# Optimization experiments

Hardware: AMD Instinct MI355X
Metric: run time of the kernel (lower is better)

The kernel has to match this reference:

```python
import jax, jax.numpy as jnp
import numpy as np

NUM_ENT = 100000
NUM_REL = 500            # distinct relations; table holds 2*NUM_REL (forward + inverse)
E = 500000               # total edges: first half original, second half reversed
D = 200                  # init_dim = gcn_dim = embed_dim
B = 256
KW, KH = 10, 20          # ConvE reshape: 2*KW*KH == 2*D
NF, KS = 200, 7
FLAT = (2 * KW - KS + 1) * (KH - KS + 1) * NF  # 14*14*200 = 39200
EPS = 1e-5


def setup_inputs() -> dict:
    key = jax.random.key(0)
    k = jax.random.split(key, 24)
    half = E // 2
    src = jax.random.randint(k[0], (half,), 0, NUM_ENT)
    dst = jax.random.randint(k[1], (half,), 0, NUM_ENT)
    et = jax.random.randint(k[2], (half,), 0, NUM_REL)
    edge_index = jnp.stack([jnp.concatenate([src, dst]), jnp.concatenate([dst, src])])
    edge_type = jnp.concatenate([et, et + NUM_REL])
    sub = jax.random.randint(k[3], (B,), 0, NUM_ENT)
    rel = jax.random.randint(k[4], (B,), 0, 2 * NUM_REL)
    g = lambda i, shape, s=0.05: jax.random.normal(k[i], shape, jnp.float32) * s
    return dict(
        sub=sub, rel=rel, edge_index=edge_index, edge_type=edge_type,
        init_embed=g(5, (NUM_ENT, D)), init_rel=g(6, (2 * NUM_REL, D)),
        loop_rel1=g(7, (1, D)), loop_rel2=g(8, (1, D)),
        w_in1=g(9, (D, D)), w_out1=g(10, (D, D)), w_loop1=g(11, (D, D)), w_rel1=g(12, (D, D)), b1=jnp.zeros((D,), jnp.float32),
        w_in2=g(13, (D, D)), w_out2=g(14, (D, D)), w_loop2=g(15, (D, D)), w_rel2=g(16, (D, D)), b2=jnp.zeros((D,), jnp.float32),
        conv_w=g(17, (NF, 1, KS, KS)), conv_b=jnp.zeros((NF,), jnp.float32),
        bn0_g=jnp.ones((1,), jnp.float32), bn0_b=jnp.zeros((1,), jnp.float32),
        bn1_g=jnp.ones((NF,), jnp.float32), bn1_b=jnp.zeros((NF,), jnp.float32),
        bn2_g=jnp.ones((D,), jnp.float32), bn2_b=jnp.zeros((D,), jnp.float32),
        fc_w=g(18, (FLAT, D)), fc_b=jnp.zeros((D,), jnp.float32),
        ent_bias=jnp.zeros((NUM_ENT,), jnp.float32),
    )


def _bn2d(x, g, b):  # eval-mode BN: running mean 0, running var 1
    s = g / jnp.sqrt(1.0 + EPS)
    return x * s[None, :, None, None] + b[None, :, None, None]


def _bn1d(x, g, b):
    return x * (g / jnp.sqrt(1.0 + EPS)) + b


def _agg(x_src, rel_e, dst, w):
    # message = comp(h_src, h_rel) @ W   (subtraction composition), degree-normalized scatter
    m = (x_src - rel_e) @ w                                        # [E/2, D]
    s = jax.ops.segment_sum(m, dst, num_segments=NUM_ENT)          # [N, D]
    deg = jax.ops.segment_sum(jnp.ones(dst.shape, m.dtype), dst, num_segments=NUM_ENT)
    return s / jnp.clip(deg, 1.0)[:, None]


def _ragcn_layer(x, r, ei, et, w_in, w_out, w_loop, w_rel, loop_rel, b):
    half = ei.shape[1] // 2
    src, dst = ei[0], ei[1]
    re = r[et]                                                     # [E, D]
    res = (_agg(x[src[:half]], re[:half], dst[:half], w_in)
           + _agg(x[src[half:]], re[half:], dst[half:], w_out)
           + (x - loop_rel) @ w_loop)
    return jnp.tanh(res / 3.0 + b), r @ w_rel


def _forward(sub, rel, edge_index, edge_type, init_embed, init_rel,
             loop_rel1, loop_rel2, w_in1, w_out1, w_loop1, w_rel1, b1,
             w_in2, w_out2, w_loop2, w_rel2, b2, conv_w, conv_b,
             bn0_g, bn0_b, bn1_g, bn1_b, bn2_g, bn2_b, fc_w, fc_b, ent_bias):
    x, r = _ragcn_layer(init_embed, init_rel, edge_index, edge_type, w_in1, w_out1, w_loop1, w_rel1, loop_rel1, b1)
    x, r = _ragcn_layer(x, r, edge_index, edge_type, w_in2, w_out2, w_loop2, w_rel2, loop_rel2, b2)
    sub_emb = x[sub]                                               # [B, D]
    rel_emb = r[rel]                                               # [B, D]
    # ConvE concat: [B,2,D] -> [B,D,2] -> [B,1,2*KW,KH]
    stk = jnp.transpose(jnp.stack([sub_emb, rel_emb], axis=1), (0, 2, 1)).reshape(-1, 1, 2 * KW, KH)
    h = _bn2d(stk, bn0_g, bn0_b)
    h = jax.lax.conv_general_dilated(h, conv_w, (1, 1), 'VALID',
                                     dimension_numbers=('NCHW', 'OIHW', 'NCHW'))
    h = h + conv_b[None, :, None, None]
    h = jax.nn.relu(_bn2d(h, bn1_g, bn1_b))
    h = h.reshape(-1, FLAT)
    h = h @ fc_w + fc_b
    h = jax.nn.relu(_bn1d(h, bn2_g, bn2_b))
    logits = h @ x.T + ent_bias                                    # [B, NUM_ENT]
    return jax.nn.sigmoid(logits)


def reference(sub, rel, edge_index, edge_type, init_embed, init_rel,
              loop_rel1, loop_rel2, w_in1, w_out1, w_loop1, w_rel1, b1,
              w_in2, w_out2, w_loop2, w_rel2, b2, conv_w, conv_b,
              bn0_g, bn0_b, bn1_g, bn1_b, bn2_g, bn2_b, fc_w, fc_b, ent_bias):
    return _forward(sub, rel, edge_index, edge_type, init_embed, init_rel,
                    loop_rel1, loop_rel2, w_in1, w_out1, w_loop1, w_rel1, b1,
                    w_in2, w_out2, w_loop2, w_rel2, b2, conv_w, conv_b,
                    bn0_g, bn0_b, bn1_g, bn1_b, bn2_g, bn2_b, fc_w, fc_b, ent_bias)
```

## Files before the change

### kernel.cpp

```cpp
#include <hip/hip_runtime.h>
#include <math.h>

#define N_ENT   100000
#define N_REL2  1000
#define E_TOT   500000
#define E_HALF  250000
#define DIM     200
#define BB      256
#define NFILT   200
#define FLATK   39200
#define EPS_BN  1e-5f

#define NROWS   200000
#define SCHUNK  2048
#define SNBLK   ((NROWS + SCHUNK - 1) / SCHUNK)

#define FC_KC   175
#define FC_KLEN 224

typedef __attribute__((ext_vector_type(8))) short bf16x8;
typedef __attribute__((ext_vector_type(4))) float f32x4;

__device__ __forceinline__ unsigned short f2b(float f) {
    union { float f; unsigned u; } c; c.f = f;
    unsigned u = c.u;
    u += 0x7fffu + ((u >> 16) & 1u);
    return (unsigned short)(u >> 16);
}
__device__ __forceinline__ float b2f(unsigned short h) {
    union { unsigned u; float f; } c; c.u = ((unsigned)h) << 16;
    return c.f;
}
__device__ __forceinline__ float fast_tanh(float x) {
    float ax = fabsf(x);
    float e = __expf(-2.0f * ax);
    float t = (1.0f - e) / (1.0f + e);
    return copysignf(t, x);
}

__global__ void convert_kernel(const float* __restrict__ s, unsigned short* __restrict__ d,
                               int n) {
    int i = (blockIdx.x * 256 + threadIdx.x) * 4;
    if (i + 3 < n) {
        float4 v = *(const float4*)(s + i);
        ushort4 o;
        o.x = f2b(v.x); o.y = f2b(v.y); o.z = f2b(v.z); o.w = f2b(v.w);
        *(ushort4*)(d + i) = o;
    } else {
        for (; i < n; ++i) d[i] = f2b(s[i]);
    }
}

__global__ void wstack_kernel(const float* __restrict__ wIn, const float* __restrict__ wOut,
                              const float* __restrict__ wLoop, unsigned short* __restrict__ WTK) {
    int g = blockIdx.x * 256 + threadIdx.x;
    if (g >= 3 * 28 * 224 * 8) return;
    int kk = g & 7;
    int t = g >> 3;
    int col = t % 224;
    int t2 = t / 224;
    int unit = t2 % 28;
    int seg = t2 / 28;
    int k = unit * 8 + kk;
    float v = 0.f;
    if (col < 200 && k < 200)
        v = (seg == 0 ? wIn : seg == 1 ? wOut : wLoop)[k * 200 + col];
    WTK[g] = f2b(v);
}

__global__ void fwt_kernel(const float* __restrict__ fw, unsigned short* __restrict__ FWT) {
    __shared__ float t[32][33];
    const int bid = blockIdx.x;
    const int kt = bid % 1225, jt = bid / 1225;
    const int tid = threadIdx.x;
#pragma unroll
    for (int it = 0; it < 4; ++it) {
        int idx = tid + it * 256;
        int kk = idx >> 5, jj = idx & 31;
        int j = jt * 32 + jj;
        t[kk][jj] = (j < 200) ? fw[(size_t)(kt * 32 + kk) * 200 + j] : 0.f;
    }
    __syncthreads();
#pragma unroll
    for (int it = 0; it < 4; ++it) {
        int idx = tid + it * 256;
        int jj = idx >> 5, kk = idx & 31;
        int j = jt * 32 + jj;
        if (j < 208)
            FWT[(size_t)j * FLATK + kt * 32 + kk] = f2b(t[kk][jj]);
    }
}

__global__ void hist_kernel(const int* __restrict__ ei, int* __restrict__ cnt) {
    int e = blockIdx.x * 256 + threadIdx.x;
    if (e >= E_TOT) return;
    int row = ei[E_TOT + e] + (e < E_HALF ? 0 : N_ENT);
    atomicAdd(&cnt[row], 1);
}

__global__ void scan1_kernel(const int* __restrict__ cnt, int* __restrict__ row_start,
                             int* __restrict__ blockSum) {
    __shared__ int tsum[256];
    const int t = threadIdx.x;
    const int base = blockIdx.x * SCHUNK + t * 8;
    int v[8];
    int s = 0;
#pragma unroll
    for (int i = 0; i < 8; ++i) {
        int idx = base + i;
        int c = (idx < NROWS) ? cnt[idx] : 0;
        v[i] = s;
        s += c;
    }
    tsum[t] = s;
    __syncthreads();
    for (int off = 1; off < 256; off <<= 1) {
        int x = (t >= off) ? tsum[t - off] : 0;
        __syncthreads();
        if (t >= off) tsum[t] += x;
        __syncthreads();
    }
    int texc = (t == 0) ? 0 : tsum[t - 1];
    if (t == 0) blockSum[blockIdx.x] = tsum[255];
#pragma unroll
    for (int i = 0; i < 8; ++i) {
        int idx = base + i;
        if (idx < NROWS) row_start[idx] = texc + v[i];
    }
}

__global__ void scan2_kernel(int* __restrict__ blockSum) {
    int s = 0;
    for (int i = 0; i < SNBLK; ++i) { int c = blockSum[i]; blockSum[i] = s; s += c; }
}

__global__ void scan3_kernel(int* __restrict__ row_start, int* __restrict__ row_cur,
                             const int* __restrict__ blockSum) {
    int i = blockIdx.x * 256 + threadIdx.x;
    if (i >= NROWS) return;
    int v = row_start[i] + blockSum[i / SCHUNK];
    row_start[i] = v;
    row_cur[i] = v;
}

__global__ void fill_kernel(const int* __restrict__ ei, const int* __restrict__ et,
                            int* __restrict__ row_cur, int2* __restrict__ epair) {
    int e = blockIdx.x * 256 + threadIdx.x;
    if (e >= E_TOT) return;
    int row = ei[E_TOT + e] + (e < E_HALF ? 0 : N_ENT);
    int pos = atomicAdd(&row_cur[row], 1);
    epair[pos] = make_int2(ei[e], et[e]);
}

__global__ void gather_kernel(const unsigned short* __restrict__ x,
                              const unsigned short* __restrict__ r,
                              const int2* __restrict__ epair,
                              const int* __restrict__ row_start, const int* __restrict__ cnt,
                              unsigned short* __restrict__ agg) {
    int wid = blockIdx.x * 4 + (threadIdx.x >> 6);
    if (wid >= NROWS) return;
    int lane = threadIdx.x & 63;
    if (lane >= 50) return;
    int start = row_start[wid];
    int deg = cnt[wid];
    float a0 = 0.f, a1 = 0.f, a2 = 0.f, a3 = 0.f;
    float c0 = 0.f, c1 = 0.f, c2 = 0.f, c3 = 0.f;
    int i = 0;
    for (; i + 2 <= deg; i += 2) {
        int2 e0 = epair[start + i];
        int2 e1 = epair[start + i + 1];
        ushort4 xv0 = *(const ushort4*)(x + (size_t)e0.x * DIM + lane * 4);
        ushort4 rv0 = *(const ushort4*)(r + (size_t)e0.y * DIM + lane * 4);
        ushort4 xv1 = *(const ushort4*)(x + (size_t)e1.x * DIM + lane * 4);
        ushort4 rv1 = *(const ushort4*)(r + (size_t)e1.y * DIM + lane * 4);
        a0 += b2f(xv0.x) - b2f(rv0.x);
        a1 += b2f(xv0.y) - b2f(rv0.y);
        a2 += b2f(xv0.z) - b2f(rv0.z);
        a3 += b2f(xv0.w) - b2f(rv0.w);
        c0 += b2f(xv1.x) - b2f(rv1.x);
        c1 += b2f(xv1.y) - b2f(rv1.y);
        c2 += b2f(xv1.z) - b2f(rv1.z);
        c3 += b2f(xv1.w) - b2f(rv1.w);
    }
    if (i < deg) {
        int2 e = epair[start + i];
        ushort4 xv = *(const ushort4*)(x + (size_t)e.x * DIM + lane * 4);
        ushort4 rv = *(const ushort4*)(r + (size_t)e.y * DIM + lane * 4);
        a0 += b2f(xv.x) - b2f(rv.x);
        a1 += b2f(xv.y) - b2f(rv.y);
        a2 += b2f(xv.z) - b2f(rv.z);
        a3 += b2f(xv.w) - b2f(rv.w);
    }
    float sc = 1.0f / fmaxf((float)deg, 1.0f);
    ushort4 o;
    o.x = f2b((a0 + c0) * sc);
    o.y = f2b((a1 + c1) * sc);
    o.z = f2b((a2 + c2) * sc);
    o.w = f2b((a3 + c3) * sc);
    *(ushort4*)(agg + (size_t)wid * DIM + lane * 4) = o;
}

__global__ void lv_kernel(const float* __restrict__ lr, const float* __restrict__ wl,
                          float* __restrict__ lv) {
    int j = blockIdx.x * blockDim.x + threadIdx.x;
    if (j >= DIM) return;
    float acc = 0.f;
    for (int k = 0; k < DIM; ++k) acc += lr[k] * wl[k * DIM + j];
    lv[j] = acc;
}

__global__ void rgemm_kernel(const float* __restrict__ r, const float* __restrict__ w,
                             float* __restrict__ out, int rows) {
    int g = blockIdx.x * 256 + threadIdx.x;
    if (g >= rows * DIM) return;
    int i = g / DIM, j = g - i * DIM;
    float acc = 0.f;
    for (int k = 0; k < DIM; ++k) acc += r[i * DIM + k] * w[k * DIM + j];
    out[g] = acc;
}

#define LOAD_A2(g, buf) do {                                                    \
    const unsigned short* Ap_ = Aseg[(g) / 7];                                  \
    const unsigned short* base_ = Ap_ + (size_t)arow * 200 + ((g) % 7) * 32 + lq * 8; \
    buf[0] = *(const bf16x8*)(base_);                                           \
    buf[1] = *(const bf16x8*)(base_ + 16 * 200);                                \
} while (0)

__global__ __launch_bounds__(256, 4) void layer_mfma_kernel(
        const unsigned short* __restrict__ aggI, const unsigned short* __restrict__ aggO,
        const unsigned short* __restrict__ xin, const unsigned short* __restrict__ WTK,
        const float* __restrict__ lv, const float* __restrict__ bias,
        unsigned short* __restrict__ out, int nwg) {
    __shared__ unsigned short Wl[16 * 112 * 8];
    const int bid = blockIdx.x;
    const int q = nwg >> 3, rr = nwg & 7;
    const int xcd = bid & 7, idx = bid >> 3;
    const int L = (xcd < rr ? xcd * (q + 1) : rr * (q + 1) + (xcd - rr) * q) + idx;
    const int rowblk  = L >> 1;
    const int colbase = (L & 1) * 112;

    const int tid  = threadIdx.x;
    const int wm   = tid >> 6;
    const int lane = tid & 63;
    const int lr   = lane & 15;
    const int lq   = lane >> 4;
    const int row0 = rowblk * 128;
    const int arow = row0 + wm * 32 + lr;

    const unsigned short* const Aseg[3] = { aggI, aggO, xin };

    f32x4 acc[2][7];
#pragma unroll
    for (int m = 0; m < 2; ++m)
#pragma unroll
        for (int n = 0; n < 7; ++n) acc[m][n] = (f32x4){0.f, 0.f, 0.f, 0.f};

    bf16x8 apf[3][2];
    LOAD_A2(0, apf[0]);
    LOAD_A2(1, apf[1]);

#pragma unroll
    for (int seg = 0; seg < 3; ++seg) {
#pragma unroll
        for (int ph = 0; ph < 2; ++ph) {
            if (seg + ph) __syncthreads();
            if (ph == 0) {
#pragma unroll
                for (int it = 0; it < 7; ++it) {
                    int u = tid + it * 256;
                    int unit = u / 112, col = u - unit * 112;
                    *(int4*)(&Wl[(unit * 112 + col) * 8]) =
                        *(const int4*)(WTK + ((size_t)(seg * 28 + unit) * 224 + colbase + col) * 8);
                }
            } else {
                for (int u = tid; u < 1344; u += 256) {
                    int unit = u / 112, col = u - unit * 112;
                    *(int4*)(&Wl[(unit * 112 + col) * 8]) =
                        *(const int4*)(WTK + ((size_t)(seg * 28 + 16 + unit) * 224 + colbase + col) * 8);
                }
            }
            __syncthreads();
            const int NC = (ph == 0) ? 4 : 3;
#pragma unroll
            for (int cc = 0; cc < NC; ++cc) {
                const int g = seg * 7 + (ph ? 4 : 0) + cc;
                if (g + 2 < 21) LOAD_A2(g + 2, apf[(g + 2) % 3]);
#pragma unroll
                for (int n = 0; n < 7; ++n) {
                    bf16x8 b = *(const bf16x8*)(&Wl[((cc * 4 + lq) * 112 + n * 16 + lr) * 8]);
                    acc[0][n] = __builtin_amdgcn_mfma_f32_16x16x32_bf16(apf[g % 3][0], b, acc[0][n], 0, 0, 0);
                    acc[1][n] = __builtin_amdgcn_mfma_f32_16x16x32_bf16(apf[g % 3][1], b, acc[1][n], 0, 0, 0);
                }
            }
        }
    }

#pragma unroll
    for (int m = 0; m < 2; ++m) {
        int rbase = row0 + wm * 32 + m * 16 + lq * 4;
#pragma unroll
        for (int n = 0; n < 7; ++n) {
            int col = colbase + n * 16 + lr;
            if (col < 200) {
                float lvc = lv[col], bc = bias[col];
#pragma unroll
                for (int r2 = 0; r2 < 4; ++r2) {
                    int row = rbase + r2;
                    if (row < N_ENT) {
                        float v = (acc[m][n][r2] - lvc) * (1.0f / 3.0f) + bc;
                        out[(size_t)row * 200 + col] = f2b(fast_tanh(v));
                    }
                }
            }
        }
    }
}

__global__ void img_kernel(const unsigned short* __restrict__ x, const float* __restrict__ r,
                           const int* __restrict__ sub, const int* __restrict__ rel,
                           const float* __restrict__ bn0g, const float* __restrict__ bn0b,
                           unsigned short* __restrict__ img) {
    int g = blockIdx.x * 256 + threadIdx.x;
    if (g >= BB * 2 * DIM) return;
    int b = g / 400, l = g - b * 400;
    int d = l >> 1;
    float v = (l & 1) ? r[(size_t)rel[b] * DIM + d] : b2f(x[(size_t)sub[b] * DIM + d]);
    float s0 = bn0g[0] * rsqrtf(1.0f + EPS_BN);
    img[g] = f2b(v * s0 + bn0b[0]);
}

__global__ void im2col_kernel(const unsigned short* __restrict__ img,
                              unsigned short* __restrict__ IM) {
    int g = blockIdx.x * 256 + threadIdx.x;
    if (g >= 50176 * 64) return;
    int row = g >> 6, k = g & 63;
    int b = row / 196, p = row - b * 196;
    int h = p / 14, w = p - h * 14;
    unsigned short v = 0;
    if (k < 49) {
        int i = k / 7, j = k - i * 7;
        v = img[b * 400 + (h + i) * 20 + (w + j)];
    }
    IM[g] = v;
}

__global__ void cwt_kernel(const float* __restrict__ cw, unsigned short* __restrict__ CWT) {
    int g = blockIdx.x * 256 + threadIdx.x;
    if (g >= 208 * 64) return;
    int f = g >> 6, k = g & 63;
    CWT[g] = (f < 200 && k < 49) ? f2b(cw[f * 49 + k]) : 0;
}

__global__ __launch_bounds__(256) void conv_mfma_kernel(
        const unsigned short* __restrict__ IM, const unsigned short* __restrict__ CWT,
        const float* __restrict__ cb, const float* __restrict__ bn1g,
        const float* __restrict__ bn1b, unsigned short* __restrict__ CO_B) {
    const int tid  = threadIdx.x;
    const int row0 = blockIdx.x * 128;
    const int wave = tid >> 6;
    const int lane = tid & 63;
    const int lr   = lane & 15;
    const int lq   = lane >> 4;
    const int arow = row0 + wave * 32 + lr;

    f32x4 acc[2][13];
#pragma unroll
    for (int m = 0; m < 2; ++m)
#pragma unroll
        for (int n = 0; n < 13; ++n) acc[m][n] = (f32x4){0.f, 0.f, 0.f, 0.f};

#pragma unroll
    for (int c = 0; c < 2; ++c) {
        const int k = c * 32 + lq * 8;
        bf16x8 a0 = *(const bf16x8*)(IM + (size_t)arow * 64 + k);
        bf16x8 a1 = *(const bf16x8*)(IM + (size_t)(arow + 16) * 64 + k);
#pragma unroll
        for (int n = 0; n < 13; ++n) {
            bf16x8 b = *(const bf16x8*)(CWT + (size_t)(n * 16 + lr) * 64 + k);
            acc[0][n] = __builtin_amdgcn_mfma_f32_16x16x32_bf16(a0, b, acc[0][n], 0, 0, 0);
            acc[1][n] = __builtin_amdgcn_mfma_f32_16x16x32_bf16(a1, b, acc[1][n], 0, 0, 0);
        }
    }

#pragma unroll
    for (int m = 0; m < 2; ++m) {
        int grow_base = row0 + wave * 32 + m * 16 + lq * 4;
#pragma unroll
        for (int n = 0; n < 13; ++n) {
            int col = n * 16 + lr;
            if (col < 200) {
                float s1 = bn1g[col] * rsqrtf(1.0f + EPS_BN);
                float t1 = bn1b[col];
                float cbf = cb[col];
#pragma unroll
                for (int r = 0; r < 4; ++r) {
                    int grow = grow_base + r;
                    int b = grow / 196, p = grow - b * 196;
                    float v = fmaxf((acc[m][n][r] + cbf) * s1 + t1, 0.f);
                    CO_B[(size_t)b * FLATK + col * 196 + p] = f2b(v);
                }
            }
        }
    }
}

__global__ __launch_bounds__(256) void fc_mfma_kernel(
        const unsigned short* __restrict__ CO_B, const unsigned short* __restrict__ FWT,
        float* __restrict__ partials) {
    const int tid  = threadIdx.x;
    const int kc   = blockIdx.x >> 2;
    const int mb   = blockIdx.x & 3;
    const int wave = tid >> 6;
    const int lane = tid & 63;
    const int lr   = lane & 15;
    const int lq   = lane >> 4;
    const int m0   = mb * 64 + wave * 16;

    f32x4 acc[13];
#pragma unroll
    for (int n = 0; n < 13; ++n) acc[n] = (f32x4){0.f, 0.f, 0.f, 0.f};

#pragma unroll
    for (int s = 0; s < 7; ++s) {
        const int k = kc * FC_KLEN + s * 32 + lq * 8;
        bf16x8 a = *(const bf16x8*)(CO_B + (size_t)(m0 + lr) * FLATK + k);
#pragma unroll
        for (int n = 0; n < 13; ++n) {
            bf16x8 b = *(const bf16x8*)(FWT + (size_t)(n * 16 + lr) * FLATK + k);
            acc[n] = __builtin_amdgcn_mfma_f32_16x16x32_bf16(a, b, acc[n], 0, 0, 0);
        }
    }

    float* slab = partials + (size_t)kc * (BB * 208);
#pragma unroll
    for (int n = 0; n < 13; ++n) {
        int col = n * 16 + lr;
#pragma unroll
        for (int r = 0; r < 4; ++r) {
            int row = m0 + lq * 4 + r;
            slab[(size_t)row * 208 + col] = acc[n][r];
        }
    }
}

__global__ void fc_reduce_kernel(const float* __restrict__ partials,
                                 const float* __restrict__ fcb,
                                 const float* __restrict__ g2, const float* __restrict__ b2v,
                                 unsigned short* __restrict__ hb) {
    int g = blockIdx.x * 256 + threadIdx.x;
    if (g >= BB * 224) return;
    int b = g / 224, j = g - b * 224;
    unsigned short o = 0;
    if (j < 200) {
        float s = 0.f;
        const float* p = partials + (size_t)b * 208 + j;
#pragma unroll 5
        for (int c = 0; c < FC_KC; ++c)
            s += p[(size_t)c * (BB * 208)];
        float v = (s + fcb[j]) * (g2[j] * rsqrtf(1.0f + EPS_BN)) + b2v[j];
        o = f2b(fmaxf(v, 0.f));
    }
    hb[g] = o;
}

#define LOAD_HB(g, buf) do {                                                    \
    const unsigned short* base_ = hb + (size_t)brow * 224 + (g) * 32 + lq * 8;  \
    buf[0] = *(const bf16x8*)(base_);                                           \
    buf[1] = *(const bf16x8*)(base_ + 16 * 224);                                \
} while (0)

__global__ __launch_bounds__(512, 2) void logits_mfma_kernel(
        const unsigned short* __restrict__ x, const unsigned short* __restrict__ hb,
        const float* __restrict__ eb, float* __restrict__ out, int nwg) {
    __shared__ unsigned short Xl[112 * 136];
    const int bid = blockIdx.x;
    const int q = nwg >> 3, rr = nwg & 7;
    const int xcd = bid & 7, idx = bid >> 3;
    const int nb = (xcd < rr ? xcd * (q + 1) : rr * (q + 1) + (xcd - rr) * q) + idx;
    const int ent0 = nb * 112;

    const int tid  = threadIdx.x;
    const int wave = tid >> 6;
    const int mh   = wave >> 2;
    const int wm   = wave & 3;
    const int lane = tid & 63;
    const int lr   = lane & 15;
    const int lq   = lane >> 4;
    const int brow = mh * 128 + wm * 32 + lr;

    f32x4 acc[2][7];
#pragma unroll
    for (int m = 0; m < 2; ++m)
#pragma unroll
        for (int n = 0; n < 7; ++n) acc[m][n] = (f32x4){0.f, 0.f, 0.f, 0.f};

    bf16x8 apf[3][2];
    LOAD_HB(0, apf[0]);
    LOAD_HB(1, apf[1]);

#pragma unroll
    for (int ph = 0; ph < 2; ++ph) {
        if (ph) __syncthreads();
        if (ph == 0) {
#pragma unroll
            for (int it = 0; it < 4; ++it) {
                int u = tid + it * 512;
                if (u < 1792) {
                    int row = u >> 4, c = u & 15;
                    int ent = ent0 + row;
                    int4 v = make_int4(0, 0, 0, 0);
                    if (ent < N_ENT)
                        v = *(const int4*)(x + (size_t)ent * 200 + c * 8);
                    *(int4*)(&Xl[row * 136 + c * 8]) = v;
                }
            }
        } else {
            for (int u = tid; u < 1344; u += 512) {
                int row = u / 12, c = u - row * 12;
                int gu = 16 + c;
                int ent = ent0 + row;
                int4 v = make_int4(0, 0, 0, 0);
                if (ent < N_ENT && gu < 25)
                    v = *(const int4*)(x + (size_t)ent * 200 + gu * 8);
                *(int4*)(&Xl[row * 136 + c * 8]) = v;
            }
        }
        __syncthreads();
        const int NC = (ph == 0) ? 4 : 3;
#pragma unroll
        for (int cc = 0; cc < NC; ++cc) {
            const int g = (ph ? 4 : 0) + cc;
            if (g + 2 < 7) LOAD_HB(g + 2, apf[(g + 2) % 3]);
#pragma unroll
            for (int n = 0; n < 7; ++n) {
                bf16x8 b = *(const bf16x8*)(&Xl[(n * 16 + lr) * 136 + cc * 32 + lq * 8]);
                acc[0][n] = __builtin_amdgcn_mfma_f32_16x16x32_bf16(apf[g % 3][0], b, acc[0][n], 0, 0, 0);
                acc[1][n] = __builtin_amdgcn_mfma_f32_16x16x32_bf16(apf[g % 3][1], b, acc[1][n], 0, 0, 0);
            }
        }
    }

#pragma unroll
    for (int m = 0; m < 2; ++m) {
        int b_base = mh * 128 + wm * 32 + m * 16 + lq * 4;
#pragma unroll
        for (int n = 0; n < 7; ++n) {
            int ent = ent0 + n * 16 + lr;
            if (ent < N_ENT) {
                float bias = eb[ent];
#pragma unroll
                for (int r = 0; r < 4; ++r) {
                    float v = acc[m][n][r] + bias;
                    out[(size_t)(b_base + r) * N_ENT + ent] = 1.0f / (1.0f + __expf(-v));
                }
            }
        }
    }
}

extern "C" void kernel_launch(void* const* d_in, const int* in_sizes, int n_in,
                              void* d_out, int out_size, void* d_ws, size_t ws_size,
                              hipStream_t stream) {
    const int*   sub        = (const int*)  d_in[0];
    const int*   rel        = (const int*)  d_in[1];
    const int*   edge_index = (const int*)  d_in[2];
    const int*   edge_type  = (const int*)  d_in[3];
    const float* init_embed = (const float*)d_in[4];
    const float* init_rel   = (const float*)d_in[5];
    const float* loop_rel1  = (const float*)d_in[6];
    const float* loop_rel2  = (const float*)d_in[7];
    const float* w_in1      = (const float*)d_in[8];
    const float* w_out1     = (const float*)d_in[9];
    const float* w_loop1    = (const float*)d_in[10];
    const float* w_rel1     = (const float*)d_in[11];
    const float* b1         = (const float*)d_in[12];
    const float* w_in2      = (const float*)d_in[13];
    const float* w_out2     = (const float*)d_in[14];
    const float* w_loop2    = (const float*)d_in[15];
    const float* w_rel2     = (const float*)d_in[16];
    const float* b2         = (const float*)d_in[17];
    const float* conv_w     = (const float*)d_in[18];
    const float* conv_b     = (const float*)d_in[19];
    const float* bn0_g      = (const float*)d_in[20];
    const float* bn0_b      = (const float*)d_in[21];
    const float* bn1_g      = (const float*)d_in[22];
    const float* bn1_b      = (const float*)d_in[23];
    const float* bn2_g      = (const float*)d_in[24];
    const float* bn2_b      = (const float*)d_in[25];
    const float* fc_w       = (const float*)d_in[26];
    const float* fc_b       = (const float*)d_in[27];
    const float* ent_bias   = (const float*)d_in[28];

    unsigned short* aggb = (unsigned short*)d_ws;
    unsigned short* x0b  = aggb + 40000000;
    unsigned short* x1b  = x0b  + 20000000;
    unsigned short* r0b  = x1b  + 20000000;
    unsigned short* r1b  = r0b  + 200000;
    unsigned short* WTK  = r1b  + 200000;
    unsigned short* img  = WTK  + 150528;
    unsigned short* IM   = img  + 102400;
    unsigned short* CWT  = IM   + 3211264;
    unsigned short* CO_B = CWT  + 13312;
    unsigned short* hb16 = CO_B + 10035200;
    unsigned short* FWT  = hb16 + 57344;
    float* fbase = (float*)(FWT + 8153600);
    float* r1f      = fbase;
    float* r2f      = r1f  + 200000;
    float* lv       = r2f  + 200000;
    float* partials = lv   + 256;

    int2* epair    = (int2*)CO_B;
    int* cnt       = (int*)(epair + E_TOT);
    int* row_start = cnt  + NROWS;
    int* row_cur   = row_start + NROWS;
    int* blockSum  = row_cur + NROWS;

    unsigned short* aggIb = aggb;
    unsigned short* aggOb = aggb + (size_t)N_ENT * DIM;
    unsigned short* x2b   = x0b;

    const int gather_blocks = (NROWS + 3) / 4;
    const int layer_nwg     = ((N_ENT + 127) / 128) * 2;
    const int logits_nwg    = (N_ENT + 111) / 112;
    const int wstack_blocks = (3 * 28 * 224 * 8 + 255) / 256;

    convert_kernel<<<(N_ENT * DIM + 1023) / 1024, 256, 0, stream>>>(init_embed, x0b, N_ENT * DIM);
    convert_kernel<<<(N_REL2 * DIM + 1023) / 1024, 256, 0, stream>>>(init_rel, r0b, N_REL2 * DIM);
    hipMemsetAsync(cnt, 0, (size_t)NROWS * 4, stream);
    hist_kernel<<<(E_TOT + 255) / 256, 256, 0, stream>>>(edge_index, cnt);
    scan1_kernel<<<SNBLK, 256, 0, stream>>>(cnt, row_start, blockSum);
    scan2_kernel<<<1, 1, 0, stream>>>(blockSum);
    scan3_kernel<<<(NROWS + 255) / 256, 256, 0, stream>>>(row_start, row_cur, blockSum);
    fill_kernel<<<(E_TOT + 255) / 256, 256, 0, stream>>>(edge_index, edge_type, row_cur, epair);

    wstack_kernel<<<wstack_blocks, 256, 0, stream>>>(w_in1, w_out1, w_loop1, WTK);
    gather_kernel<<<gather_blocks, 256, 0, stream>>>(x0b, r0b, epair, row_start, cnt, aggb);
    lv_kernel<<<1, 256, 0, stream>>>(loop_rel1, w_loop1, lv);
    layer_mfma_kernel<<<layer_nwg, 256, 0, stream>>>(aggIb, aggOb, x0b, WTK, lv, b1, x1b, layer_nwg);
    rgemm_kernel<<<(N_REL2 * DIM + 255) / 256, 256, 0, stream>>>(init_rel, w_rel1, r1f, N_REL2);
    convert_kernel<<<(N_REL2 * DIM + 1023) / 1024, 256, 0, stream>>>(r1f, r1b, N_REL2 * DIM);

    wstack_kernel<<<wstack_blocks, 256, 0, stream>>>(w_in2, w_out2, w_loop2, WTK);
    gather_kernel<<<gather_blocks, 256, 0, stream>>>(x1b, r1b, epair, row_start, cnt, aggb);
    lv_kernel<<<1, 256, 0, stream>>>(loop_rel2, w_loop2, lv);
    layer_mfma_kernel<<<layer_nwg, 256, 0, stream>>>(aggIb, aggOb, x1b, WTK, lv, b2, x2b, layer_nwg);
    rgemm_kernel<<<(N_REL2 * DIM + 255) / 256, 256, 0, stream>>>(r1f, w_rel2, r2f, N_REL2);

    img_kernel<<<(BB * 400 + 255) / 256, 256, 0, stream>>>(x2b, r2f, sub, rel,
                                                           bn0_g, bn0_b, img);
    im2col_kernel<<<(50176 * 64 + 255) / 256, 256, 0, stream>>>(img, IM);
    cwt_kernel<<<(208 * 64 + 255) / 256, 256, 0, stream>>>(conv_w, CWT);
    conv_mfma_kernel<<<50176 / 128, 256, 0, stream>>>(IM, CWT, conv_b, bn1_g, bn1_b, CO_B);
    fwt_kernel<<<1225 * 7, 256, 0, stream>>>(fc_w, FWT);
    fc_mfma_kernel<<<FC_KC * 4, 256, 0, stream>>>(CO_B, FWT, partials);
    fc_reduce_kernel<<<(BB * 224 + 255) / 256, 256, 0, stream>>>(partials, fc_b, bn2_g, bn2_b, hb16);

    logits_mfma_kernel<<<logits_nwg, 512, 0, stream>>>(x2b, hb16, ent_bias, (float*)d_out,
                                                       logits_nwg);
}
```

Measured before the change: 604.0 us.

## Halve layer GEMM row tile to 64 and deepen A prefetch

The layer MFMA kernel now gives each workgroup 64 rows instead of 128, so each wave computes one 16-row M tile rather than two. The grid doubles, launch bounds ask for 5 waves per SIMD, the A-operand prefetch goes from 2 to 3 chunks ahead, and MFMA sections run at raised wave priority. The aim is more occupancy and parallelism to hide global load latency. The cost is that each W tile staged in LDS is reused over half as many rows, so W is loaded and synchronized twice as often per output row.

Measured after the change: 588.2 us. 2.6% less time.

```diff
diff --git a/kernel.cpp b/kernel.cpp
--- a/kernel.cpp
+++ b/kernel.cpp
@@ -219,14 +219,12 @@
     out[g] = acc;
 }
 
-#define LOAD_A2(g, buf) do {                                                    \
+#define LOAD_A1(g, slot) do {                                                   \
     const unsigned short* Ap_ = Aseg[(g) / 7];                                  \
-    const unsigned short* base_ = Ap_ + (size_t)arow * 200 + ((g) % 7) * 32 + lq * 8; \
-    buf[0] = *(const bf16x8*)(base_);                                           \
-    buf[1] = *(const bf16x8*)(base_ + 16 * 200);                                \
+    apf[slot] = *(const bf16x8*)(Ap_ + (size_t)arow * 200 + ((g) % 7) * 32 + lq * 8); \
 } while (0)
 
-__global__ __launch_bounds__(256, 4) void layer_mfma_kernel(
+__global__ __launch_bounds__(256, 5) void layer_mfma_kernel(
         const unsigned short* __restrict__ aggI, const unsigned short* __restrict__ aggO,
         const unsigned short* __restrict__ xin, const unsigned short* __restrict__ WTK,
         const float* __restrict__ lv, const float* __restrict__ bias,
@@ -244,20 +242,19 @@
     const int lane = tid & 63;
     const int lr   = lane & 15;
     const int lq   = lane >> 4;
-    const int row0 = rowblk * 128;
-    const int arow = row0 + wm * 32 + lr;
+    const int row0 = rowblk * 64;
+    const int arow = row0 + wm * 16 + lr;
 
     const unsigned short* const Aseg[3] = { aggI, aggO, xin };
 
-    f32x4 acc[2][7];
-#pragma unroll
-    for (int m = 0; m < 2; ++m)
-#pragma unroll
-        for (int n = 0; n < 7; ++n) acc[m][n] = (f32x4){0.f, 0.f, 0.f, 0.f};
-
-    bf16x8 apf[3][2];
-    LOAD_A2(0, apf[0]);
-    LOAD_A2(1, apf[1]);
+    f32x4 acc[7];
+#pragma unroll
+    for (int n = 0; n < 7; ++n) acc[n] = (f32x4){0.f, 0.f, 0.f, 0.f};
+
+    bf16x8 apf[4];
+    LOAD_A1(0, 0);
+    LOAD_A1(1, 1);
+    LOAD_A1(2, 2);
 
 #pragma unroll
     for (int seg = 0; seg < 3; ++seg) {
@@ -268,7 +265,8 @@
 #pragma unroll
                 for (int it = 0; it < 7; ++it) {
                     int u = tid + it * 256;
-                    int unit = u / 112, col = u - unit * 112;
+                    int unit = u >> 7 , col;
+                    unit = u / 112; col = u - unit * 112;
                     *(int4*)(&Wl[(unit * 112 + col) * 8]) =
                         *(const int4*)(WTK + ((size_t)(seg * 28 + unit) * 224 + colbase + col) * 8);
                 }
@@ -284,20 +282,20 @@
 #pragma unroll
             for (int cc = 0; cc < NC; ++cc) {
                 const int g = seg * 7 + (ph ? 4 : 0) + cc;
-                if (g + 2 < 21) LOAD_A2(g + 2, apf[(g + 2) % 3]);
+                if (g + 3 < 21) LOAD_A1(g + 3, (g + 3) & 3);
+                __builtin_amdgcn_s_setprio(1);
 #pragma unroll
                 for (int n = 0; n < 7; ++n) {
                     bf16x8 b = *(const bf16x8*)(&Wl[((cc * 4 + lq) * 112 + n * 16 + lr) * 8]);
-                    acc[0][n] = __builtin_amdgcn_mfma_f32_16x16x32_bf16(apf[g % 3][0], b, acc[0][n], 0, 0, 0);
-                    acc[1][n] = __builtin_amdgcn_mfma_f32_16x16x32_bf16(apf[g % 3][1], b, acc[1][n], 0, 0, 0);
+                    acc[n] = __builtin_amdgcn_mfma_f32_16x16x32_bf16(apf[g & 3], b, acc[n], 0, 0, 0);
                 }
-            }
-        }
-    }
-
-#pragma unroll
-    for (int m = 0; m < 2; ++m) {
-        int rbase = row0 + wm * 32 + m * 16 + lq * 4;
+                __builtin_amdgcn_s_setprio(0);
+            }
+        }
+    }
+
+    {
+        int rbase = row0 + wm * 16 + lq * 4;
 #pragma unroll
         for (int n = 0; n < 7; ++n) {
             int col = colbase + n * 16 + lr;
@@ -307,7 +305,7 @@
                 for (int r2 = 0; r2 < 4; ++r2) {
                     int row = rbase + r2;
                     if (row < N_ENT) {
-                        float v = (acc[m][n][r2] - lvc) * (1.0f / 3.0f) + bc;
+                        float v = (acc[n][r2] - lvc) * (1.0f / 3.0f) + bc;
                         out[(size_t)row * 200 + col] = f2b(fast_tanh(v));
                     }
                 }
@@ -620,7 +618,7 @@
     unsigned short* x2b   = x0b;
 
     const int gather_blocks = (NROWS + 3) / 4;
-    const int layer_nwg     = ((N_ENT + 127) / 128) * 2;
+    const int layer_nwg     = ((N_ENT + 63) / 64) * 2;
     const int logits_nwg    = (N_ENT + 111) / 112;
     const int wstack_blocks = (3 * 28 * 224 * 8 + 255) / 256;
 
```
